# Performance work log

Hardware: AMD Instinct MI355X
Metric: run time of the kernel (lower is better)

The kernel has to match this reference:

```python
import jax, jax.numpy as jnp
import numpy as np
import math

PHI = (1.0 + math.sqrt(5.0)) / 2.0
LN_EPS = 1e-5


def _carrier_phases(n_heads: int) -> np.ndarray:
    """Reproduce DimensionalHeadManager._allocate carrier phases."""
    base = [k * math.pi / 7.0 for k in range(7)]  # rung base phases
    n_rungs = 7
    raw = []
    remaining = n_heads
    for i in range(n_rungs):
        if i < n_rungs - 1:
            c = max(1, round(n_heads / PHI ** (i + 1)))
            c = min(c, remaining - (n_rungs - 1 - i))
            raw.append(c)
            remaining -= c
        else:
            raw.append(max(1, remaining))
    phases = []
    for rung_idx, count in enumerate(raw):
        for j in range(count):
            phases.append(base[rung_idx] + 2.0 * math.pi / max(count, 1) * j)
    return np.asarray(phases[:n_heads], dtype=np.float32)


def setup_inputs() -> dict:
    key = jax.random.key(0)
    ks = jax.random.split(key, 7)
    B, S, D, H = 2, 2048, 1024, 16
    w_scale = 0.02  # realistic init scale for Linear weights
    x = jax.random.normal(ks[0], (B, S, D), dtype=jnp.float32)
    Wq = jax.random.normal(ks[1], (D, D), dtype=jnp.float32) * w_scale
    Wk = jax.random.normal(ks[2], (D, D), dtype=jnp.float32) * w_scale
    Wv = jax.random.normal(ks[3], (D, D), dtype=jnp.float32) * w_scale
    Wo = jax.random.normal(ks[4], (D, D), dtype=jnp.float32) * w_scale
    Wp = jax.random.normal(ks[5], (D,), dtype=jnp.float32) * w_scale  # W_phase (1,D) flattened
    gamma = jnp.ones((D,), dtype=jnp.float32)
    beta = jnp.zeros((D,), dtype=jnp.float32)
    carrier = jnp.asarray(_carrier_phases(H))  # srl.carrier_freq init
    lam = jnp.float32(0.1)  # lambda_resonance init
    return {"x": x, "Wq": Wq, "Wk": Wk, "Wv": Wv, "Wo": Wo, "Wp": Wp,
            "gamma": gamma, "beta": beta, "carrier": carrier, "lam": lam}


def reference(x, Wq, Wk, Wv, Wo, Wp, gamma, beta, carrier, lam):
    B, S, D = x.shape
    H = carrier.shape[0]
    dh = D // H
    scale = 1.0 / math.sqrt(dh)

    residual = x
    # LayerNorm
    mu = jnp.mean(x, axis=-1, keepdims=True)
    var = jnp.mean((x - mu) ** 2, axis=-1, keepdims=True)
    xn = (x - mu) * jax.lax.rsqrt(var + LN_EPS) * gamma + beta

    # Q/K/V projections (torch Linear: y = x @ W.T), split into heads
    q = jnp.einsum('bsd,ed->bse', xn, Wq).reshape(B, S, H, dh)
    k = jnp.einsum('bsd,ed->bse', xn, Wk).reshape(B, S, H, dh)
    v = jnp.einsum('bsd,ed->bse', xn, Wv).reshape(B, S, H, dh)

    # scalar phase per token, per-head carrier resonance gate
    phase = jnp.einsum('bsd,d->bs', xn, Wp)                       # (B,S)
    head_T = jnp.cos((phase[..., None] - carrier) * 0.5) ** 2     # (B,S,H)

    # attention scores + resonance term R_ij = cos^2((phi_i - phi_j)/2)
    scores = jnp.einsum('bihd,bjhd->bhij', q, k) * scale          # (B,H,S,S)
    R = jnp.cos((phase[:, :, None] - phase[:, None, :]) * 0.5) ** 2  # (B,S,S)
    scores = scores + lam * R[:, None, :, :]

    attn = jax.nn.softmax(scores, axis=-1)
    out = jnp.einsum('bhij,bjhd->bihd', attn, v)                  # (B,S,H,dh)
    out = out * head_T[..., None]                                 # per-head resonance gating
    emergent_energy = jnp.sum(jnp.abs(out))
    y = residual + jnp.einsum('bse,de->bsd', out.reshape(B, S, D), Wo)
    return (y, emergent_energy)
```

## Files before the change

kernel.cpp:

```cpp
#include <hip/hip_runtime.h>
#include <hip/hip_bf16.h>

#define S_LEN 2048
#define D_MODEL 1024
#define NH 16
#define DH 64
#define M_TOK 4096
#define DK 80

typedef __attribute__((ext_vector_type(8))) short bf16x8;
typedef __attribute__((ext_vector_type(4))) float f32x4;
typedef __attribute__((ext_vector_type(16))) float f32x16;

#define LOG2E 1.4426950408889634f

__device__ __forceinline__ unsigned short f2bf(float f) {
  unsigned u = __float_as_uint(f);
  u += 0x7FFF + ((u >> 16) & 1);
  return (unsigned short)(u >> 16);
}

__device__ __forceinline__ void gl16(const void* g, void* l) {
  __builtin_amdgcn_global_load_lds(
      (const __attribute__((address_space(1))) unsigned int*)g,
      (__attribute__((address_space(3))) unsigned int*)l, 16, 0, 0);
}

__global__ __launch_bounds__(256) void prep_kernel(
    const float* __restrict__ Wq, const float* __restrict__ Wk,
    const float* __restrict__ Wv, const float* __restrict__ Wo,
    unsigned short* __restrict__ wbf, float* __restrict__ energy) {
  if (blockIdx.x == 0 && threadIdx.x == 0) *energy = 0.f;
  int idx = (blockIdx.x * 256 + threadIdx.x) * 4;
  int wsel = idx >> 20;
  const float* s = (wsel == 0) ? Wq : (wsel == 1) ? Wk : (wsel == 2) ? Wv : Wo;
  int off = idx & 1048575;
  float4 v = *(const float4*)(s + off);
  ushort4 p;
  p.x = f2bf(v.x); p.y = f2bf(v.y); p.z = f2bf(v.z); p.w = f2bf(v.w);
  *(ushort4*)(wbf + idx) = p;
}

__device__ __forceinline__ float block_sum(float v, float* sm) {
#pragma unroll
  for (int o = 32; o > 0; o >>= 1) v += __shfl_xor(v, o, 64);
  int w = threadIdx.x >> 6;
  __syncthreads();
  if ((threadIdx.x & 63) == 0) sm[w] = v;
  __syncthreads();
  return sm[0] + sm[1] + sm[2] + sm[3];
}

__global__ __launch_bounds__(256) void ln_phase_kernel(
    const float* __restrict__ x, const float* __restrict__ Wp,
    const float* __restrict__ gamma, const float* __restrict__ beta,
    unsigned short* __restrict__ xn, float* __restrict__ cosP,
    float* __restrict__ sinP) {
  __shared__ float sm[4];
  int row = blockIdx.x;
  int tid = threadIdx.x;
  float4 v = ((const float4*)(x + (size_t)row * D_MODEL))[tid];
  float mu = block_sum(v.x + v.y + v.z + v.w, sm) * (1.0f / D_MODEL);
  float d0 = v.x - mu, d1 = v.y - mu, d2 = v.z - mu, d3 = v.w - mu;
  float var = block_sum(d0 * d0 + d1 * d1 + d2 * d2 + d3 * d3, sm) * (1.0f / D_MODEL);
  float rinv = rsqrtf(var + 1e-5f);
  float4 g = ((const float4*)gamma)[tid];
  float4 be = ((const float4*)beta)[tid];
  float n0 = d0 * rinv * g.x + be.x;
  float n1 = d1 * rinv * g.y + be.y;
  float n2 = d2 * rinv * g.z + be.z;
  float n3 = d3 * rinv * g.w + be.w;
  ushort4 p;
  p.x = f2bf(n0); p.y = f2bf(n1); p.z = f2bf(n2); p.w = f2bf(n3);
  ((ushort4*)(xn + (size_t)row * D_MODEL))[tid] = p;
  float4 wp = ((const float4*)Wp)[tid];
  float ph = block_sum(n0 * wp.x + n1 * wp.y + n2 * wp.z + n3 * wp.w, sm);
  if (tid == 0) {
    cosP[row] = cosf(ph);
    sinP[row] = sinf(ph);
  }
}

__global__ __launch_bounds__(256) void phase_fill_kernel(
    const float* __restrict__ cosP, const float* __restrict__ sinP,
    unsigned short* __restrict__ kk80) {
  int gid = blockIdx.x * 256 + threadIdx.x;
  int s = gid & (S_LEN - 1);
  int bh = gid >> 11;
  int b = bh >> 4;
  int tok = b * S_LEN + s;
  unsigned int w0 = (unsigned int)f2bf(cosP[tok]) | ((unsigned int)f2bf(sinP[tok]) << 16);
  *(int4*)(kk80 + (size_t)gid * DK + 64) = make_int4((int)w0, 0, 0, 0);
}

__global__ __launch_bounds__(256, 3) void qkv_gemm_kernel(
    const unsigned short* __restrict__ xn, const unsigned short* __restrict__ wbf,
    unsigned short* __restrict__ q, unsigned short* __restrict__ kk80,
    unsigned short* __restrict__ vT) {
  __shared__ __align__(16) unsigned short As[128 * 64];
  __shared__ __align__(16) unsigned short Bs[128 * 64];
  int bid = blockIdx.x;
  bool vmode = bid >= 512;
  const unsigned short* Ap;
  const unsigned short* Bp;
  int m0, n0;
  if (!vmode) {
    m0 = (bid >> 4) * 128;
    n0 = (bid & 15) * 128;
    Ap = xn; Bp = wbf;
  } else {
    int v2 = bid - 512;
    m0 = (v2 & 7) * 128;
    n0 = (v2 >> 3) * 128;
    Ap = wbf + 2 * D_MODEL * D_MODEL; Bp = xn;
  }
  int tid = threadIdx.x;
  int wave = tid >> 6, lane = tid & 63, quad = lane >> 4, l15 = lane & 15;
  int wm = (wave & 1) * 64, wn = (wave >> 1) * 64;
  f32x4 acc[4][4];
#pragma unroll
  for (int r = 0; r < 4; ++r)
#pragma unroll
    for (int c = 0; c < 4; ++c) acc[r][c] = (f32x4){0.f, 0.f, 0.f, 0.f};

  for (int k0 = 0; k0 < D_MODEL; k0 += 64) {
    __syncthreads();
#pragma unroll
    for (int t = 0; t < 4; ++t) {
      int c = t * 256 + tid;
      int r = c >> 3, p = c & 7;
      int g = p ^ (r & 7);
      gl16(&Ap[(size_t)(m0 + r) * D_MODEL + k0 + g * 8], &As[c * 8]);
      gl16(&Bp[(size_t)(n0 + r) * D_MODEL + k0 + g * 8], &Bs[c * 8]);
    }
    __syncthreads();
    bf16x8 af[4][2], bfr[4][2];
#pragma unroll
    for (int r = 0; r < 4; ++r) {
      int R = wm + r * 16 + l15;
#pragma unroll
      for (int h = 0; h < 2; ++h)
        af[r][h] = *(const bf16x8*)&As[R * 64 + ((h * 4 + quad) ^ (R & 7)) * 8];
    }
#pragma unroll
    for (int c = 0; c < 4; ++c) {
      int R = wn + c * 16 + l15;
#pragma unroll
      for (int h = 0; h < 2; ++h)
        bfr[c][h] = *(const bf16x8*)&Bs[R * 64 + ((h * 4 + quad) ^ (R & 7)) * 8];
    }
#pragma unroll
    for (int h = 0; h < 2; ++h)
#pragma unroll
      for (int r = 0; r < 4; ++r)
#pragma unroll
        for (int c = 0; c < 4; ++c)
          acc[r][c] = __builtin_amdgcn_mfma_f32_16x16x32_bf16(af[r][h], bfr[c][h], acc[r][c], 0, 0, 0);
  }
#pragma unroll
  for (int r = 0; r < 4; ++r) {
#pragma unroll
    for (int c = 0; c < 4; ++c) {
#pragma unroll
      for (int rr = 0; rr < 4; ++rr) {
        if (vmode) {
          int e = m0 + wm + r * 16 + quad * 4 + rr;
          int tok = n0 + wn + c * 16 + l15;
          int hh = e >> 6, d = e & 63;
          int bb = tok >> 11, ss = tok & (S_LEN - 1);
          vT[(((size_t)(bb * NH + hh)) * DH + d) * S_LEN + ss] = f2bf(acc[r][c][rr]);
        } else {
          int tok = m0 + wm + r * 16 + quad * 4 + rr;
          int n = n0 + wn + c * 16 + l15;
          int e = n & 1023;
          int hh = e >> 6, d = e & 63;
          int bb = tok >> 11, ss = tok & (S_LEN - 1);
          if ((n0 >> 10) == 0) {
            q[(((size_t)(bb * NH + hh)) * S_LEN + ss) * DH + d] =
                f2bf(acc[r][c][rr] * (0.125f * LOG2E));
          } else {
            kk80[(((size_t)(bb * NH + hh)) * S_LEN + ss) * DK + d] = f2bf(acc[r][c][rr]);
          }
        }
      }
    }
  }
}

__global__ __launch_bounds__(128, 3) void attn_kernel(
    const unsigned short* __restrict__ q, const unsigned short* __restrict__ kk80,
    const unsigned short* __restrict__ vT, const float* __restrict__ cosP,
    const float* __restrict__ sinP, const float* __restrict__ carrier,
    const float* __restrict__ lamp, unsigned short* __restrict__ outw,
    float* __restrict__ energy) {
  __shared__ __align__(16) unsigned short Ks[64 * 72];
  __shared__ __align__(16) unsigned short Vs[512 * 8];
  __shared__ __align__(16) unsigned int Ps[2][32 * 34];
  __shared__ float Lr[2][32];
  __shared__ float er[2];
  int qt = blockIdx.x, h = blockIdx.y, b = blockIdx.z;
  int bh = b * NH + h;
  int tid = threadIdx.x, wave = tid >> 6, lane = tid & 63;
  int half = lane >> 5, l31 = lane & 31;

  const unsigned short* kb = kk80 + (size_t)bh * S_LEN * DK;
  const unsigned short* vb = vT + (size_t)bh * DH * S_LEN;
  int qrow = qt * 64 + wave * 32 + l31;

  bf16x8 bQ[5];
  {
    const unsigned short* qp = q + ((size_t)bh * S_LEN + qrow) * DH;
#pragma unroll
    for (int db = 0; db < 4; ++db)
      bQ[db] = *(const bf16x8*)(qp + db * 16 + half * 8);
    bf16x8 z8 = {0, 0, 0, 0, 0, 0, 0, 0};
    if (half == 0) {
      float hl2 = 0.5f * lamp[0] * LOG2E;
      z8[0] = (short)f2bf(hl2 * cosP[b * S_LEN + qrow]);
      z8[1] = (short)f2bf(hl2 * sinP[b * S_LEN + qrow]);
    }
    bQ[4] = z8;
  }

  f32x16 O0 = {}, O1 = {};
  float l_i = 0.f;

  for (int j0 = 0; j0 < S_LEN; j0 += 64) {
    __syncthreads();
#pragma unroll
    for (int t = 0; t < 4; ++t) {
      unsigned int cc = t * 128 + tid;
      unsigned int r = cc / 9u, p = cc - r * 9u;
      gl16(&kb[(size_t)(j0 + r) * DK + p * 8], (unsigned short*)Ks + cc * 8);
    }
    if (tid < 64) {
      unsigned int cc = 512 + tid;
      unsigned int r = cc / 9u, p = cc - r * 9u;
      gl16(&kb[(size_t)(j0 + r) * DK + p * 8], (unsigned short*)Ks + cc * 8);
    }
#pragma unroll
    for (int t = 0; t < 4; ++t) {
      int cc = t * 128 + tid;
      int r = cc >> 3, p = cc & 7;
      int g = p ^ (r & 7);
      gl16(&vb[(size_t)r * S_LEN + j0 + g * 8], (unsigned short*)Vs + cc * 8);
    }
    __syncthreads();

    f32x16 Sf[2];
#pragma unroll
    for (int sj = 0; sj < 2; ++sj) {
      Sf[sj] = (f32x16){};
      int r = sj * 32 + l31;
#pragma unroll
      for (int db = 0; db < 5; ++db) {
        int p = (db < 4) ? (db * 2 + half) : 8;
        bf16x8 aK = *(const bf16x8*)((const unsigned short*)Ks + (r * 9 + p) * 8);
        Sf[sj] = __builtin_amdgcn_mfma_f32_32x32x16_bf16(aK, bQ[db], Sf[sj], 0, 0, 0);
      }
    }

#pragma unroll
    for (int sj = 0; sj < 2; ++sj) {
#pragma unroll
      for (int rr = 0; rr < 8; ++rr) {
        float e0 = exp2f(Sf[sj][rr * 2 + 0]);
        float e1 = exp2f(Sf[sj][rr * 2 + 1]);
        l_i += e0 + e1;
        __hip_bfloat162 pk = __float22bfloat162_rn(float2{e0, e1});
        int jd = sj * 16 + (rr >> 1) * 4 + half * 2 + (rr & 1);
        Ps[wave][l31 * 34 + jd] = *(unsigned int*)&pk;
      }
    }

#pragma unroll
    for (int jb = 0; jb < 4; ++jb) {
      const unsigned int* pp = &Ps[wave][l31 * 34 + jb * 8 + half * 4];
      uint2 a0 = *(const uint2*)pp;
      uint2 a1 = *(const uint2*)(pp + 2);
      union { unsigned int u[4]; bf16x8 v; } cvt;
      cvt.u[0] = a0.x; cvt.u[1] = a0.y; cvt.u[2] = a1.x; cvt.u[3] = a1.y;
      {
        int rv = l31;
        int p = (jb * 2 + half) ^ (rv & 7);
        bf16x8 bV = *(const bf16x8*)((const unsigned short*)Vs + (rv * 8 + p) * 8);
        O0 = __builtin_amdgcn_mfma_f32_32x32x16_bf16(cvt.v, bV, O0, 0, 0, 0);
      }
      {
        int rv = 32 + l31;
        int p = (jb * 2 + half) ^ (rv & 7);
        bf16x8 bV = *(const bf16x8*)((const unsigned short*)Vs + (rv * 8 + p) * 8);
        O1 = __builtin_amdgcn_mfma_f32_32x32x16_bf16(cvt.v, bV, O1, 0, 0, 0);
      }
    }
  }

  l_i += __shfl_xor(l_i, 32, 64);
  Lr[wave][l31] = l_i;
  float ch = cosf(carrier[h]), sh = sinf(carrier[h]);
  float esum = 0.f;
#pragma unroll
  for (int reg = 0; reg < 16; ++reg) {
    int ir = (reg & 3) + 8 * (reg >> 2) + 4 * half;
    int srow = qt * 64 + wave * 32 + ir;
    float cp = cosP[b * S_LEN + srow], sp = sinP[b * S_LEN + srow];
    float gate = 0.5f + 0.5f * (cp * ch + sp * sh);
    float gl = gate / Lr[wave][ir];
    float v0 = O0[reg] * gl, v1 = O1[reg] * gl;
    esum += fabsf(v0) + fabsf(v1);
    size_t tok = (size_t)b * S_LEN + srow;
    outw[tok * D_MODEL + h * DH + l31] = f2bf(v0);
    outw[tok * D_MODEL + h * DH + 32 + l31] = f2bf(v1);
  }
#pragma unroll
  for (int off = 32; off > 0; off >>= 1) esum += __shfl_xor(esum, off, 64);
  if (lane == 0) er[wave] = esum;
  __syncthreads();
  if (tid == 0) atomicAdd(energy, er[0] + er[1]);
}

__global__ __launch_bounds__(256) void out_gemm_kernel(
    const unsigned short* __restrict__ A, const unsigned short* __restrict__ Wo,
    const float* __restrict__ x, float* __restrict__ y) {
  __shared__ __align__(16) unsigned short As[128 * 64];
  __shared__ __align__(16) unsigned short Bs[64 * 64];
  int tid = threadIdx.x;
  int wave = tid >> 6, lane = tid & 63, quad = lane >> 4, l15 = lane & 15;
  int wm = (wave & 1) * 64, wn = (wave >> 1) * 32;
  int m0 = blockIdx.y * 128, n0 = blockIdx.x * 64;
  f32x4 acc[4][2];
#pragma unroll
  for (int r = 0; r < 4; ++r)
#pragma unroll
    for (int c = 0; c < 2; ++c) acc[r][c] = (f32x4){0.f, 0.f, 0.f, 0.f};

  for (int k0 = 0; k0 < D_MODEL; k0 += 64) {
    __syncthreads();
#pragma unroll
    for (int t = 0; t < 4; ++t) {
      int c = t * 256 + tid;
      int r = c >> 3, p = c & 7;
      int qc = p ^ (r & 7);
      gl16(&A[(size_t)(m0 + r) * D_MODEL + k0 + qc * 8], &As[c * 8]);
    }
#pragma unroll
    for (int t = 0; t < 2; ++t) {
      int c = t * 256 + tid;
      int r = c >> 3, p = c & 7;
      int qc = p ^ (r & 7);
      gl16(&Wo[(size_t)(n0 + r) * D_MODEL + k0 + qc * 8], &Bs[c * 8]);
    }
    __syncthreads();
    bf16x8 af[4][2], bfr[2][2];
#pragma unroll
    for (int r = 0; r < 4; ++r) {
      int R = wm + r * 16 + l15;
#pragma unroll
      for (int h = 0; h < 2; ++h)
        af[r][h] = *(const bf16x8*)&As[R * 64 + ((h * 4 + quad) ^ (R & 7)) * 8];
    }
#pragma unroll
    for (int c = 0; c < 2; ++c) {
      int R = wn + c * 16 + l15;
#pragma unroll
      for (int h = 0; h < 2; ++h)
        bfr[c][h] = *(const bf16x8*)&Bs[R * 64 + ((h * 4 + quad) ^ (R & 7)) * 8];
    }
#pragma unroll
    for (int h = 0; h < 2; ++h)
#pragma unroll
      for (int r = 0; r < 4; ++r)
#pragma unroll
        for (int c = 0; c < 2; ++c)
          acc[r][c] = __builtin_amdgcn_mfma_f32_16x16x32_bf16(af[r][h], bfr[c][h], acc[r][c], 0, 0, 0);
  }
#pragma unroll
  for (int r = 0; r < 4; ++r) {
#pragma unroll
    for (int c = 0; c < 2; ++c) {
      int dcol = n0 + wn + c * 16 + l15;
#pragma unroll
      for (int rr = 0; rr < 4; ++rr) {
        int tok = m0 + wm + r * 16 + quad * 4 + rr;
        size_t idx = (size_t)tok * D_MODEL + dcol;
        y[idx] = x[idx] + acc[r][c][rr];
      }
    }
  }
}

extern "C" void kernel_launch(void* const* d_in, const int* in_sizes, int n_in,
                              void* d_out, int out_size, void* d_ws, size_t ws_size,
                              hipStream_t stream) {
  const float* x = (const float*)d_in[0];
  const float* Wq = (const float*)d_in[1];
  const float* Wk = (const float*)d_in[2];
  const float* Wv = (const float*)d_in[3];
  const float* Wo = (const float*)d_in[4];
  const float* Wp = (const float*)d_in[5];
  const float* gamma = (const float*)d_in[6];
  const float* beta = (const float*)d_in[7];
  const float* carrier = (const float*)d_in[8];
  const float* lam = (const float*)d_in[9];

  char* ws = (char*)d_ws;
  const size_t MB = 1024 * 1024;
  unsigned short* wbf = (unsigned short*)(ws);
  unsigned short* xn = (unsigned short*)(ws + 8 * MB);
  unsigned short* qq = (unsigned short*)(ws + 16 * MB);
  unsigned short* kk80 = (unsigned short*)(ws + 24 * MB);
  unsigned short* vT = (unsigned short*)(ws + 34 * MB);
  float* cosP = (float*)(ws + 42 * MB);
  float* sinP = (float*)(ws + 42 * MB + 16 * 1024);
  unsigned short* outw = xn;

  float* y = (float*)d_out;
  float* energy = y + (out_size - 1);

  prep_kernel<<<4096, 256, 0, stream>>>(Wq, Wk, Wv, Wo, wbf, energy);
  ln_phase_kernel<<<M_TOK, 256, 0, stream>>>(x, Wp, gamma, beta, xn, cosP, sinP);
  phase_fill_kernel<<<256, 256, 0, stream>>>(cosP, sinP, kk80);
  qkv_gemm_kernel<<<768, 256, 0, stream>>>(xn, wbf, qq, kk80, vT);
  attn_kernel<<<dim3(32, 16, 2), 128, 0, stream>>>(qq, kk80, vT, cosP, sinP,
                                                   carrier, lam, outw, energy);
  out_gemm_kernel<<<dim3(16, 32), 256, 0, stream>>>(outw, wbf + 3 * D_MODEL * D_MODEL,
                                                    x, y);
}
```

Before: 232.8 us.

## Double-buffer K/V tiles and keep P in registers via permlane32 swap

The attention loop now double-buffers the K and V LDS tiles, so the next tile's global-to-LDS load is issued before computing on the current one, with one barrier per iteration instead of two. The probability matrix P no longer round-trips through LDS. It is repacked in registers with v_permlane32_swap into the MFMA operand layout. s_setprio is raised around the MFMA groups. The extra LDS buffers lower the occupancy hint from 3 to 2 blocks per CU, which may reduce latency hiding.

```diff
diff --git a/kernel.cpp b/kernel.cpp
--- a/kernel.cpp
+++ b/kernel.cpp
@@ -24,6 +24,10 @@
   __builtin_amdgcn_global_load_lds(
       (const __attribute__((address_space(1))) unsigned int*)g,
       (__attribute__((address_space(3))) unsigned int*)l, 16, 0, 0);
+}
+
+__device__ __forceinline__ void pl32swap(unsigned int& a, unsigned int& b) {
+  asm volatile("v_permlane32_swap_b32 %0, %1" : "+v"(a), "+v"(b));
 }
 
 __global__ __launch_bounds__(256) void prep_kernel(
@@ -187,15 +191,14 @@
   }
 }
 
-__global__ __launch_bounds__(128, 3) void attn_kernel(
+__global__ __launch_bounds__(128, 2) void attn_kernel(
     const unsigned short* __restrict__ q, const unsigned short* __restrict__ kk80,
     const unsigned short* __restrict__ vT, const float* __restrict__ cosP,
     const float* __restrict__ sinP, const float* __restrict__ carrier,
     const float* __restrict__ lamp, unsigned short* __restrict__ outw,
     float* __restrict__ energy) {
-  __shared__ __align__(16) unsigned short Ks[64 * 72];
-  __shared__ __align__(16) unsigned short Vs[512 * 8];
-  __shared__ __align__(16) unsigned int Ps[2][32 * 34];
+  __shared__ __align__(16) unsigned short Ks[2][64 * 72];
+  __shared__ __align__(16) unsigned short Vs[2][512 * 8];
   __shared__ float Lr[2][32];
   __shared__ float er[2];
   int qt = blockIdx.x, h = blockIdx.y, b = blockIdx.z;
@@ -225,74 +228,93 @@
   f32x16 O0 = {}, O1 = {};
   float l_i = 0.f;
 
-  for (int j0 = 0; j0 < S_LEN; j0 += 64) {
-    __syncthreads();
+  auto stage = [&](int bi, int jbase) {
+    unsigned short* ksd = &Ks[bi][0];
+    unsigned short* vsd = &Vs[bi][0];
 #pragma unroll
     for (int t = 0; t < 4; ++t) {
       unsigned int cc = t * 128 + tid;
       unsigned int r = cc / 9u, p = cc - r * 9u;
-      gl16(&kb[(size_t)(j0 + r) * DK + p * 8], (unsigned short*)Ks + cc * 8);
+      gl16(&kb[(size_t)(jbase + r) * DK + p * 8], ksd + cc * 8);
     }
     if (tid < 64) {
       unsigned int cc = 512 + tid;
       unsigned int r = cc / 9u, p = cc - r * 9u;
-      gl16(&kb[(size_t)(j0 + r) * DK + p * 8], (unsigned short*)Ks + cc * 8);
+      gl16(&kb[(size_t)(jbase + r) * DK + p * 8], ksd + cc * 8);
     }
 #pragma unroll
     for (int t = 0; t < 4; ++t) {
       int cc = t * 128 + tid;
       int r = cc >> 3, p = cc & 7;
       int g = p ^ (r & 7);
-      gl16(&vb[(size_t)r * S_LEN + j0 + g * 8], (unsigned short*)Vs + cc * 8);
-    }
-    __syncthreads();
+      gl16(&vb[(size_t)r * S_LEN + jbase + g * 8], vsd + cc * 8);
+    }
+  };
+
+  int cur = 0;
+  stage(0, 0);
+  __syncthreads();
+
+  for (int jt = 0; jt < 32; ++jt) {
+    if (jt < 31) stage(cur ^ 1, (jt + 1) * 64);
+
+    const unsigned short* ksb = &Ks[cur][0];
+    const unsigned short* vsb = &Vs[cur][0];
 
     f32x16 Sf[2];
 #pragma unroll
     for (int sj = 0; sj < 2; ++sj) {
       Sf[sj] = (f32x16){};
       int r = sj * 32 + l31;
+      __builtin_amdgcn_s_setprio(1);
 #pragma unroll
       for (int db = 0; db < 5; ++db) {
         int p = (db < 4) ? (db * 2 + half) : 8;
-        bf16x8 aK = *(const bf16x8*)((const unsigned short*)Ks + (r * 9 + p) * 8);
+        bf16x8 aK = *(const bf16x8*)(ksb + (r * 9 + p) * 8);
         Sf[sj] = __builtin_amdgcn_mfma_f32_32x32x16_bf16(aK, bQ[db], Sf[sj], 0, 0, 0);
       }
+      __builtin_amdgcn_s_setprio(0);
     }
 
 #pragma unroll
     for (int sj = 0; sj < 2; ++sj) {
+      unsigned int w[8];
 #pragma unroll
       for (int rr = 0; rr < 8; ++rr) {
         float e0 = exp2f(Sf[sj][rr * 2 + 0]);
         float e1 = exp2f(Sf[sj][rr * 2 + 1]);
         l_i += e0 + e1;
-        __hip_bfloat162 pk = __float22bfloat162_rn(float2{e0, e1});
-        int jd = sj * 16 + (rr >> 1) * 4 + half * 2 + (rr & 1);
-        Ps[wave][l31 * 34 + jd] = *(unsigned int*)&pk;
+        __hip_bfloat162 pk2 = __float22bfloat162_rn(float2{e0, e1});
+        w[rr] = *(unsigned int*)&pk2;
       }
-    }
-
-#pragma unroll
-    for (int jb = 0; jb < 4; ++jb) {
-      const unsigned int* pp = &Ps[wave][l31 * 34 + jb * 8 + half * 4];
-      uint2 a0 = *(const uint2*)pp;
-      uint2 a1 = *(const uint2*)(pp + 2);
-      union { unsigned int u[4]; bf16x8 v; } cvt;
-      cvt.u[0] = a0.x; cvt.u[1] = a0.y; cvt.u[2] = a1.x; cvt.u[3] = a1.y;
-      {
-        int rv = l31;
-        int p = (jb * 2 + half) ^ (rv & 7);
-        bf16x8 bV = *(const bf16x8*)((const unsigned short*)Vs + (rv * 8 + p) * 8);
-        O0 = __builtin_amdgcn_mfma_f32_32x32x16_bf16(cvt.v, bV, O0, 0, 0, 0);
+#pragma unroll
+      for (int u = 0; u < 2; ++u) {
+        unsigned int a0 = w[u * 4 + 0], a1 = w[u * 4 + 1];
+        unsigned int b0 = w[u * 4 + 2], b1 = w[u * 4 + 3];
+        pl32swap(a0, b0);
+        pl32swap(a1, b1);
+        union { unsigned int u4[4]; bf16x8 v; } cvt;
+        cvt.u4[0] = a0; cvt.u4[1] = a1; cvt.u4[2] = b0; cvt.u4[3] = b1;
+        int jb = sj * 2 + u;
+        __builtin_amdgcn_s_setprio(1);
+        {
+          int rv = l31;
+          int p = (jb * 2 + half) ^ (rv & 7);
+          bf16x8 bV = *(const bf16x8*)(vsb + (rv * 8 + p) * 8);
+          O0 = __builtin_amdgcn_mfma_f32_32x32x16_bf16(cvt.v, bV, O0, 0, 0, 0);
+        }
+        {
+          int rv = 32 + l31;
+          int p = (jb * 2 + half) ^ (rv & 7);
+          bf16x8 bV = *(const bf16x8*)(vsb + (rv * 8 + p) * 8);
+          O1 = __builtin_amdgcn_mfma_f32_32x32x16_bf16(cvt.v, bV, O1, 0, 0, 0);
+        }
+        __builtin_amdgcn_s_setprio(0);
       }
-      {
-        int rv = 32 + l31;
-        int p = (jb * 2 + half) ^ (rv & 7);
-        bf16x8 bV = *(const bf16x8*)((const unsigned short*)Vs + (rv * 8 + p) * 8);
-        O1 = __builtin_amdgcn_mfma_f32_32x32x16_bf16(cvt.v, bV, O1, 0, 0, 0);
-      }
-    }
+    }
+
+    __syncthreads();
+    cur ^= 1;
   }
 
   l_i += __shfl_xor(l_i, 32, 64);
```

After: 225.6 us. 1.03x faster.
